# Performance work log

Hardware: AMD Instinct MI355X
Metric: run time of the kernel (lower is better)

The kernel has to match this reference:

```python
import jax, jax.numpy as jnp
import numpy as np

B, I, O, E, K = 32768, 256, 128, 8, 4


def _layernorm(h, g, b, eps=1e-5):
    mu = h.mean(-1, keepdims=True)
    var = h.var(-1, keepdims=True)
    return (h - mu) * jax.lax.rsqrt(var + eps) * g + b


def setup_inputs():
    key = jax.random.key(0)
    ks = iter(jax.random.split(key, 40))
    def w(shape, scale=0.02):
        return jax.random.normal(next(ks), shape, dtype=jnp.float32) * scale
    inp = {
        'x': jax.random.normal(next(ks), (B, I), dtype=jnp.float32),
        'modality_id': jax.random.randint(next(ks), (B,), 0, 3, dtype=jnp.int32),
        # experts 0-1: Linear-ReLU-Linear (stacked over leading expert dim)
        'A_W1': w((2, O, I)), 'A_b1': w((2, O)), 'A_W2': w((2, O, O)), 'A_b2': w((2, O)),
        # experts 2-3: Linear-Tanh-BatchNorm1d(eval)-Linear
        'B_W1': w((2, O, I)), 'B_b1': w((2, O)),
        'B_g': jnp.ones((2, O), jnp.float32), 'B_be': jnp.zeros((2, O), jnp.float32),
        'B_W2': w((2, O, O)), 'B_b2': w((2, O)),
        # experts 4-5: Conv1d(1->4,k3,p1)-Flatten-Linear-GELU
        'C_cw': w((2, 4, 1, 3), 0.1), 'C_cb': w((2, 4)),
        'C_W': w((2, O, 4 * I)), 'C_b': w((2, O)),
        # experts 6-7: Linear-SiLU-LayerNorm-Linear
        'D_W1': w((2, O, I)), 'D_b1': w((2, O)),
        'D_g': jnp.ones((2, O), jnp.float32), 'D_be': jnp.zeros((2, O), jnp.float32),
        'D_W2': w((2, O, O)), 'D_b2': w((2, O)),
        # shared expert: Linear-ReLU-LayerNorm-Linear (dropout off in eval)
        'S_W1': w((O, I)), 'S_b1': w((O,)),
        'S_g': jnp.ones((O,), jnp.float32), 'S_be': jnp.zeros((O,), jnp.float32),
        'S_W2': w((O, O)), 'S_b2': w((O,)),
        # gate: Linear(I+1 -> I//2)-Tanh-Linear(-> E)
        'G_W1': w((I // 2, I + 1)), 'G_b1': w((I // 2,)),
        'G_W2': w((E, I // 2)), 'G_b2': w((E,)),
    }
    return inp


def _forward(x, modality_id, A_W1, A_b1, A_W2, A_b2, B_W1, B_b1, B_g, B_be, B_W2, B_b2,
             C_cw, C_cb, C_W, C_b, D_W1, D_b1, D_g, D_be, D_W2, D_b2,
             S_W1, S_b1, S_g, S_be, S_W2, S_b2, G_W1, G_b1, G_W2, G_b2):
    Bsz = x.shape[0]
    mod = modality_id.astype(x.dtype)[:, None]
    gate_in = jnp.concatenate([x, mod], axis=-1)                 # [B, I+1]
    gh = jnp.tanh(gate_in @ G_W1.T + G_b1)
    logits = jnp.clip((gh @ G_W2.T + G_b2) / 0.7, -10.0, 10.0)   # [B, E]
    topv, topi = jax.lax.top_k(logits, K)
    topw = jax.nn.softmax(topv, axis=-1)                          # [B, K]

    # experts 0-1
    hA = jax.nn.relu(jnp.einsum('bi,eoi->beo', x, A_W1) + A_b1)
    outA = jnp.einsum('beo,epo->bep', hA, A_W2) + A_b2
    # experts 2-3 (BatchNorm eval: running mean 0, var 1)
    hB = jnp.tanh(jnp.einsum('bi,eoi->beo', x, B_W1) + B_b1)
    hB = hB * jax.lax.rsqrt(jnp.asarray(1.0 + 1e-5, x.dtype)) * B_g + B_be
    outB = jnp.einsum('beo,epo->bep', hB, B_W2) + B_b2
    # experts 4-5
    xc = x[:, None, :]                                            # [B,1,I]
    outC = []
    for e in range(2):
        conv = jax.lax.conv_general_dilated(
            xc, C_cw[e], (1,), [(1, 1)],
            dimension_numbers=('NCH', 'OIH', 'NCH')) + C_cb[e][None, :, None]  # [B,4,I]
        flat = conv.reshape(Bsz, 4 * x.shape[1])
        outC.append(jax.nn.gelu(flat @ C_W[e].T + C_b[e], approximate=False))
    outC = jnp.stack(outC, axis=1)
    # experts 6-7
    hD = jax.nn.silu(jnp.einsum('bi,eoi->beo', x, D_W1) + D_b1)
    hD = _layernorm(hD, D_g, D_be)
    outD = jnp.einsum('beo,epo->bep', hD, D_W2) + D_b2

    expert_outputs = jnp.concatenate([outA, outB, outC, outD], axis=1)  # [B,E,O]
    picked = jnp.take_along_axis(expert_outputs, topi[:, :, None], axis=1)  # [B,K,O]
    private = jnp.sum(topw[:, :, None] * picked, axis=1)                # [B,O]

    hS = jax.nn.relu(x @ S_W1.T + S_b1)
    hS = _layernorm(hS, S_g, S_be)
    shared = hS @ S_W2.T + S_b2                                         # [B,O]

    usage = jax.nn.softmax(logits, axis=-1).mean(0)                     # [E]
    ideal = jnp.full_like(usage, 1.0 / E)
    # F.kl_div(log(usage+1e-10), ideal, reduction='batchmean') with N=E
    aux = jnp.mean(ideal * (jnp.log(ideal) - jnp.log(usage + 1e-10)))
    return shared, private, aux


def reference(x, modality_id, A_W1, A_b1, A_W2, A_b2, B_W1, B_b1, B_g, B_be, B_W2, B_b2,
              C_cw, C_cb, C_W, C_b, D_W1, D_b1, D_g, D_be, D_W2, D_b2,
              S_W1, S_b1, S_g, S_be, S_W2, S_b2, G_W1, G_b1, G_W2, G_b2):
    return _forward(x, modality_id, A_W1, A_b1, A_W2, A_b2, B_W1, B_b1, B_g, B_be, B_W2, B_b2,
                    C_cw, C_cb, C_W, C_b, D_W1, D_b1, D_g, D_be, D_W2, D_b2,
                    S_W1, S_b1, S_g, S_be, S_W2, S_b2, G_W1, G_b1, G_W2, G_b2)
```

## Files before the change

### kernel.cpp

```cpp
#include <hip/hip_runtime.h>
#include <hip/hip_bf16.h>
#include <math.h>

typedef __attribute__((ext_vector_type(8))) short short8;
typedef __attribute__((ext_vector_type(4))) float f32x4;
typedef __attribute__((ext_vector_type(4))) unsigned short us4;

#define MFMA16(a,b,c) __builtin_amdgcn_mfma_f32_16x16x32_bf16((a),(b),(c),0,0,0)

#define OFF_W1CAT   0u
#define OFF_W2CAT   589824u
#define OFF_B1      950272u
#define OFF_B2      954880u
#define OFF_LNG     958464u
#define OFF_LNB     960000u
#define OFF_BSC     961536u
#define OFF_BBI     962560u
#define OFF_USAGE   963584u
#define OFF_W8      963712u
#define OFF_W1T     2012288u

__device__ __forceinline__ unsigned short f2bf(float f) {
  union { float f; unsigned u; } v; v.f = f;
  return (unsigned short)((v.u + 0x7fffu + ((v.u >> 16) & 1u)) >> 16);
}
__device__ __forceinline__ float frcp(float x) { return __builtin_amdgcn_rcpf(x); }
__device__ __forceinline__ float ftanh(float x) {
  float ax = fabsf(x);
  float t = __expf(-2.f * ax);
  float r = (1.f - t) * frcp(1.f + t);
  return copysignf(r, x);
}
__device__ __forceinline__ float fsilu(float x) {
  return x * frcp(1.f + __expf(-x));
}
__device__ __forceinline__ float fgelu(float x) {
  float ax = fabsf(x) * 0.70710678118654752f;
  float t = frcp(fmaf(0.3275911f, ax, 1.f));
  float p = fmaf(t, 1.061405429f, -1.453152027f);
  p = fmaf(t, p, 1.421413741f);
  p = fmaf(t, p, -0.284496736f);
  p = fmaf(t, p, 0.254829592f);
  p *= t;
  float erfv = copysignf(fmaf(-p, __expf(-ax * ax), 1.f), x);
  return 0.5f * x * (1.f + erfv);
}

__global__ __launch_bounds__(256) void prep_kernel(
    const float* __restrict__ A_W1, const float* __restrict__ A_b1,
    const float* __restrict__ A_W2, const float* __restrict__ A_b2,
    const float* __restrict__ B_W1, const float* __restrict__ B_b1,
    const float* __restrict__ B_g,  const float* __restrict__ B_be,
    const float* __restrict__ B_W2, const float* __restrict__ B_b2,
    const float* __restrict__ C_cw, const float* __restrict__ C_cb,
    const float* __restrict__ C_W,  const float* __restrict__ C_b,
    const float* __restrict__ D_W1, const float* __restrict__ D_b1,
    const float* __restrict__ D_g,  const float* __restrict__ D_be,
    const float* __restrict__ D_W2, const float* __restrict__ D_b2,
    const float* __restrict__ S_W1, const float* __restrict__ S_b1,
    const float* __restrict__ S_g,  const float* __restrict__ S_be,
    const float* __restrict__ S_W2, const float* __restrict__ S_b2,
    const float* __restrict__ G_W1,
    unsigned short* __restrict__ W1cat, unsigned short* __restrict__ W2cat,
    float* __restrict__ W1T,
    float* __restrict__ b1cat, float* __restrict__ b2cat,
    float* __restrict__ lng, float* __restrict__ lnb,
    float* __restrict__ bsc, float* __restrict__ bbi,
    float* __restrict__ usage)
{
  int tid = blockIdx.x * 256 + threadIdx.x;
  if (tid < 294912) {
    int g = tid >> 15, rem = tid & 32767;
    int j = rem & 7, lane = (rem >> 3) & 63, nt = (rem >> 9) & 7, ks = rem >> 12;
    int p = nt * 16 + (lane & 15);
    int k = ks * 32 + (lane >> 4) * 8 + j;
    int src = p * 256 + k;
    float v;
    if (g < 2)      v = A_W1[g * 32768 + src];
    else if (g < 4) v = B_W1[(g - 2) * 32768 + src];
    else if (g < 6) {
      int e = g - 4;
      v = 0.f;
      for (int c = 0; c < 4; ++c)
        for (int jj = 0; jj < 3; ++jj) {
          int h = k + 1 - jj;
          if (h >= 0 && h < 256)
            v += C_cw[e*12 + c*3 + jj] * C_W[e*131072 + p*1024 + c*256 + h];
        }
    }
    else if (g < 8) v = D_W1[(g - 6) * 32768 + src];
    else            v = S_W1[src];
    W1cat[tid] = f2bf(v);
    return;
  }
  tid -= 294912;
  if (tid < 114688) {
    int g = tid >> 14, rem = tid & 16383;
    int j = rem & 7, lane = (rem >> 3) & 63, nt = (rem >> 9) & 7, ks = rem >> 12;
    int p = nt * 16 + (lane & 15);
    int k = ks * 32 + (lane >> 4) * 8 + j;
    int src = p * 128 + k;
    float v;
    if (g < 2)      v = A_W2[g * 16384 + src];
    else if (g < 4) v = B_W2[(g - 2) * 16384 + src];
    else if (g < 6) v = D_W2[(g - 4) * 16384 + src];
    else            v = S_W2[src];
    W2cat[tid] = f2bf(v);
    return;
  }
  tid -= 114688;
  if (tid < 32896) {
    int k = tid / 128, o = tid % 128;
    W1T[tid] = G_W1[o * 257 + k];
    return;
  }
  tid -= 32896;
  if (tid < 1152) {
    int g = tid / 128, p = tid % 128;
    float v;
    if (g < 2)      v = A_b1[tid];
    else if (g < 4) v = B_b1[p + (g - 2) * 128];
    else if (g < 6) v = C_b[(g - 4) * 128 + p];
    else if (g < 8) v = D_b1[p + (g - 6) * 128];
    else            v = S_b1[p];
    b1cat[tid] = v;
    return;
  }
  tid -= 1152;
  if (tid < 896) {
    int g = tid / 128, p = tid % 128;
    float v;
    if (g < 2)      v = A_b2[tid];
    else if (g < 4) v = B_b2[p + (g - 2) * 128];
    else if (g < 6) v = D_b2[p + (g - 4) * 128];
    else            v = S_b2[p];
    b2cat[tid] = v;
    return;
  }
  tid -= 896;
  if (tid < 768) {
    if (tid < 384) {
      int j = tid / 128, p = tid % 128;
      lng[tid] = (j < 2) ? D_g[tid] : S_g[p];
    } else {
      int q = tid - 384; int j = q / 128, p = q % 128;
      lnb[q] = (j < 2) ? D_be[q] : S_be[p];
    }
    return;
  }
  tid -= 768;
  if (tid < 512) {
    if (tid < 256) bsc[tid] = B_g[tid];
    else           bbi[tid - 256] = B_be[tid - 256];
    return;
  }
  tid -= 512;
  if (tid < 8) usage[tid] = 0.f;
}

__global__ __launch_bounds__(256) void prep2_kernel(
    const float* __restrict__ C_cw_unused, const float* __restrict__ C_cb,
    const float* __restrict__ C_W, float* __restrict__ b1cat)
{
  int tid = blockIdx.x * 256 + threadIdx.x;
  int e = tid >> 9, rem = tid & 511;
  int p = rem >> 2, c = rem & 3;
  const float4* row = (const float4*)(C_W + e*131072 + p*1024 + c*256);
  float s = 0.f;
  for (int q = 0; q < 64; ++q) {
    float4 v = row[q];
    s += v.x + v.y + v.z + v.w;
  }
  atomicAdd(&b1cat[(4 + e) * 128 + p], C_cb[e * 4 + c] * s);
}

__global__ __launch_bounds__(512) void gate_np_kernel(
    const float* __restrict__ x, const int* __restrict__ modality,
    const float* __restrict__ W1T, const float* __restrict__ G_b1,
    const float* __restrict__ G_W2, const float* __restrict__ G_b2,
    float* __restrict__ w8full, float* __restrict__ usage)
{
  __shared__ unsigned char Ubuf[33024];
  __shared__ float ws2[8][132];
  __shared__ float lgs[64][9];
  float* xs  = (float*)Ubuf;
  float* ghs = (float*)Ubuf;
  const int tid = threadIdx.x;
  const int wv = __builtin_amdgcn_readfirstlane(tid >> 6);
  const int lane = tid & 63;
  const int tb = blockIdx.x * 64;
  const int o0 = wv * 16;
  const int t = lane;

  for (int i = tid; i < 1024; i += 512) ws2[i >> 7][i & 127] = G_W2[i];

  float acc[16];
#pragma unroll
  for (int j = 0; j < 16; ++j) acc[j] = 0.f;

  for (int p = 0; p < 2; ++p) {
    __syncthreads();
#pragma unroll
    for (int it = 0; it < 4; ++it) {
      int f = it * 512 + tid;
      int tt = f >> 5, c4 = f & 31;
      int kk = c4 * 4;
      const float4 v = *(const float4*)(x + (size_t)(tb + tt) * 256 + p * 128 + kk);
      int col = tt ^ (((kk >> 4) & 7) << 3);
      xs[(kk + 0) * 64 + col] = v.x;
      xs[(kk + 1) * 64 + col] = v.y;
      xs[(kk + 2) * 64 + col] = v.z;
      xs[(kk + 3) * 64 + col] = v.w;
    }
    __syncthreads();
    const float* wbase = W1T + (size_t)(p * 128) * 128 + o0;
    for (int kk = 0; kk < 128; ++kk) {
      float xv = xs[kk * 64 + (t ^ (((kk >> 4) & 7) << 3))];
      const float* wk = wbase + (size_t)kk * 128;
#pragma unroll
      for (int j = 0; j < 16; ++j)
        acc[j] = fmaf(xv, wk[j], acc[j]);
    }
  }
  {
    float xv = (float)modality[tb + t];
    const float* wk = W1T + (size_t)256 * 128 + o0;
#pragma unroll
    for (int j = 0; j < 16; ++j)
      acc[j] = fmaf(xv, wk[j], acc[j]);
  }
  __syncthreads();
#pragma unroll
  for (int j = 0; j < 16; ++j)
    ghs[t * 129 + o0 + j] = (float)tanh((double)(acc[j] + G_b1[o0 + j]));
  __syncthreads();

  {
    int t2 = tid >> 3, e2 = tid & 7;
    float lg = 0.f;
    for (int o2 = 0; o2 < 128; ++o2)
      lg = fmaf(ghs[t2 * 129 + o2], ws2[e2][o2], lg);
    float s = (lg + G_b2[e2]) / 0.7f;
    lgs[t2][e2] = fminf(fmaxf(s, -10.f), 10.f);
  }
  __syncthreads();

  if (wv == 0) {
    int token = tb + lane;
    float v[8];
#pragma unroll
    for (int e = 0; e < 8; ++e) v[e] = lgs[lane][e];
    float tv[4]; int ti[4]; unsigned msk = 0;
    for (int kk = 0; kk < 4; ++kk) {
      float best = -1e30f; int bi = 0;
      for (int e = 0; e < 8; ++e)
        if (!((msk >> e) & 1u) && v[e] > best) { best = v[e]; bi = e; }
      tv[kk] = best; ti[kk] = bi; msk |= 1u << bi;
    }
    float mx = tv[0], den = 0.f, wk4[4];
#pragma unroll
    for (int kk = 0; kk < 4; ++kk) { wk4[kk] = expf(tv[kk] - mx); den += wk4[kk]; }
#pragma unroll
    for (int e = 0; e < 8; ++e) {
      float val = 0.f;
#pragma unroll
      for (int kk = 0; kk < 4; ++kk) if (ti[kk] == e) val = wk4[kk] / den;
      w8full[(size_t)token * 8 + e] = val;
    }
    float uw[8];
    float dall = 0.f, pe[8];
#pragma unroll
    for (int e = 0; e < 8; ++e) { pe[e] = expf(v[e] - mx); dall += pe[e]; }
#pragma unroll
    for (int e = 0; e < 8; ++e) uw[e] = pe[e] / dall;
    for (int m = 1; m <= 32; m <<= 1)
#pragma unroll
      for (int e = 0; e < 8; ++e) uw[e] += __shfl_xor(uw[e], m);
    if (lane == 0)
      for (int e = 0; e < 8; ++e) atomicAdd(usage + e, uw[e]);
  }
}

__global__ __launch_bounds__(512, 2) void moe_kernel(
    const float* __restrict__ x,
    const unsigned short* __restrict__ W1cat, const unsigned short* __restrict__ W2cat,
    const float* __restrict__ b1cat, const float* __restrict__ b2cat,
    const float* __restrict__ lng, const float* __restrict__ lnb,
    const float* __restrict__ bsc, const float* __restrict__ bbi,
    const float* __restrict__ w8full, float* __restrict__ out)
{
  __shared__ unsigned char smem[131072];
  short8* W1L = (short8*)smem;
  short8* W2L = (short8*)(smem + 65536);
  unsigned char* HS = smem + 98304 + (threadIdx.x >> 6) * 4096;

  const int tid = threadIdx.x;
  const int wv = tid >> 6, lane = tid & 63;
  const int l15 = lane & 15, l4 = lane >> 4;
  const int tb = blockIdx.x * 128 + wv * 16;
  const short8* W1f = (const short8*)W1cat;
  const short8* W2f = (const short8*)W2cat;

  short8 A[8];
#pragma unroll
  for (int ks = 0; ks < 8; ++ks) {
    const float* xr = x + (size_t)(tb + l15) * 256 + ks * 32 + l4 * 8;
    float4 u = *(const float4*)xr, v = *(const float4*)(xr + 4);
    short8 a;
    a[0]=(short)f2bf(u.x); a[1]=(short)f2bf(u.y); a[2]=(short)f2bf(u.z); a[3]=(short)f2bf(u.w);
    a[4]=(short)f2bf(v.x); a[5]=(short)f2bf(v.y); a[6]=(short)f2bf(v.z); a[7]=(short)f2bf(v.w);
    A[ks] = a;
  }

  f32x4 zero = {0.f, 0.f, 0.f, 0.f};
  f32x4 pacc[8];
#pragma unroll
  for (int nt = 0; nt < 8; ++nt) pacc[nt] = zero;
  const float RS = 1.0f / sqrtf(1.0f + 1e-5f);

  short8 stg[12];
#pragma unroll
  for (int i = 0; i < 8; ++i) stg[i] = W1f[tid + i * 512];
#pragma unroll
  for (int i = 0; i < 4; ++i) stg[8 + i] = W2f[tid + i * 512];

  for (int g = 0; g < 9; ++g) {
    const int type = (g < 2) ? 0 : (g < 4) ? 1 : (g < 6) ? 2 : (g < 8) ? 3 : 4;
    const int g2 = (g < 4) ? g : ((g == 8) ? 6 : g - 2);

    __syncthreads();
#pragma unroll
    for (int i = 0; i < 8; ++i) W1L[tid + i * 512] = stg[i];
#pragma unroll
    for (int i = 0; i < 4; ++i) W2L[tid + i * 512] = stg[8 + i];
    if (g < 8) {
      int gn = g + 1;
      int g2n = (gn < 4) ? gn : ((gn == 8) ? 6 : gn - 2);
#pragma unroll
      for (int i = 0; i < 8; ++i) stg[i] = W1f[(size_t)gn * 4096 + tid + i * 512];
#pragma unroll
      for (int i = 0; i < 4; ++i) stg[8 + i] = W2f[(size_t)g2n * 2048 + tid + i * 512];
    }
    __syncthreads();

    f32x4 acc[8];
#pragma unroll
    for (int nt = 0; nt < 8; ++nt) acc[nt] = zero;
#pragma unroll
    for (int ks = 0; ks < 8; ++ks)
#pragma unroll
      for (int nt = 0; nt < 8; ++nt)
        acc[nt] = MFMA16(A[ks], W1L[(ks * 8 + nt) * 64 + lane], acc[nt]);

    const float* b1 = b1cat + g * 128;

    if (type == 2) {
#pragma unroll
      for (int r = 0; r < 4; ++r) {
        float wv_ = w8full[(size_t)(tb + l4 * 4 + r) * 8 + g];
#pragma unroll
        for (int nt = 0; nt < 8; ++nt) {
          float h = fgelu(acc[nt][r] + b1[nt * 16 + l15]);
          pacc[nt][r] += wv_ * h;
        }
      }
      continue;
    }
#pragma unroll
    for (int r = 0; r < 4; ++r)
#pragma unroll
      for (int nt = 0; nt < 8; ++nt) {
        float h = acc[nt][r] + b1[nt * 16 + l15];
        if (type == 0)      h = fmaxf(h, 0.f);
        else if (type == 1) {
          int col = (g - 2) * 128 + nt * 16 + l15;
          h = ftanh(h) * RS * bsc[col] + bbi[col];
        }
        else if (type == 3) h = fsilu(h);
        else                h = fmaxf(h, 0.f);
        acc[nt][r] = h;
      }
    if (type >= 3) {
      int li = (type == 4) ? 2 : (g - 6);
#pragma unroll
      for (int r = 0; r < 4; ++r) {
        float s1 = 0.f, s2 = 0.f;
#pragma unroll
        for (int nt = 0; nt < 8; ++nt) { float h = acc[nt][r]; s1 += h; s2 += h * h; }
        for (int m = 1; m <= 8; m <<= 1) { s1 += __shfl_xor(s1, m); s2 += __shfl_xor(s2, m); }
        float mu = s1 * (1.f / 128.f);
        float var = s2 * (1.f / 128.f) - mu * mu;
        float sc = __builtin_amdgcn_rsqf(var + 1e-5f);
#pragma unroll
        for (int nt = 0; nt < 8; ++nt) {
          int col = nt * 16 + l15;
          acc[nt][r] = (acc[nt][r] - mu) * sc * lng[li * 128 + col] + lnb[li * 128 + col];
        }
      }
    }
#pragma unroll
    for (int r = 0; r < 4; ++r) {
      int row = l4 * 4 + r;
#pragma unroll
      for (int nt = 0; nt < 8; ++nt) {
        int bytecol = (nt * 16 + l15) * 2;
        int addr = row * 256 + ((((bytecol >> 4) ^ (row & 7)) << 4) | (bytecol & 15));
        *(unsigned short*)(HS + addr) = f2bf(acc[nt][r]);
      }
    }
    short8 a2[4];
#pragma unroll
    for (int ks = 0; ks < 4; ++ks) {
      int ar = l15 * 256 + ((((ks * 4 + l4) ^ (l15 & 7)) << 4));
      a2[ks] = *(const short8*)(HS + ar);
    }
    f32x4 acc2[8];
#pragma unroll
    for (int nt = 0; nt < 8; ++nt) acc2[nt] = zero;
#pragma unroll
    for (int ks = 0; ks < 4; ++ks)
#pragma unroll
      for (int nt = 0; nt < 8; ++nt)
        acc2[nt] = MFMA16(a2[ks], W2L[(ks * 8 + nt) * 64 + lane], acc2[nt]);

    const float* b2 = b2cat + g2 * 128;
    if (type == 4) {
#pragma unroll
      for (int r = 0; r < 4; ++r) {
        int token = tb + l4 * 4 + r;
#pragma unroll
        for (int nt = 0; nt < 8; ++nt)
          out[(size_t)token * 128 + nt * 16 + l15] = acc2[nt][r] + b2[nt * 16 + l15];
      }
    } else {
#pragma unroll
      for (int r = 0; r < 4; ++r) {
        float wv_ = w8full[(size_t)(tb + l4 * 4 + r) * 8 + g];
#pragma unroll
        for (int nt = 0; nt < 8; ++nt)
          pacc[nt][r] += wv_ * (acc2[nt][r] + b2[nt * 16 + l15]);
      }
    }
  }
#pragma unroll
  for (int r = 0; r < 4; ++r) {
    int token = tb + l4 * 4 + r;
#pragma unroll
    for (int nt = 0; nt < 8; ++nt)
      out[4194304 + (size_t)token * 128 + nt * 16 + l15] = pacc[nt][r];
  }
}

__global__ void aux_kernel(const float* __restrict__ usage, float* __restrict__ out) {
  if (threadIdx.x == 0 && blockIdx.x == 0) {
    float a = 0.f;
    for (int e = 0; e < 8; ++e) {
      float u = usage[e] * (1.0f / 32768.0f);
      a += 0.125f * (logf(0.125f) - logf(u + 1e-10f));
    }
    out[8388608] = a * 0.125f;
  }
}

extern "C" void kernel_launch(void* const* d_in, const int* in_sizes, int n_in,
                              void* d_out, int out_size, void* d_ws, size_t ws_size,
                              hipStream_t stream) {
  (void)in_sizes; (void)n_in; (void)out_size; (void)ws_size;
  const float* x    = (const float*)d_in[0];
  const int*   mod  = (const int*)d_in[1];
  const float* A_W1 = (const float*)d_in[2];
  const float* A_b1 = (const float*)d_in[3];
  const float* A_W2 = (const float*)d_in[4];
  const float* A_b2 = (const float*)d_in[5];
  const float* B_W1 = (const float*)d_in[6];
  const float* B_b1 = (const float*)d_in[7];
  const float* B_g  = (const float*)d_in[8];
  const float* B_be = (const float*)d_in[9];
  const float* B_W2 = (const float*)d_in[10];
  const float* B_b2 = (const float*)d_in[11];
  const float* C_cw = (const float*)d_in[12];
  const float* C_cb = (const float*)d_in[13];
  const float* C_W  = (const float*)d_in[14];
  const float* C_b  = (const float*)d_in[15];
  const float* D_W1 = (const float*)d_in[16];
  const float* D_b1 = (const float*)d_in[17];
  const float* D_g  = (const float*)d_in[18];
  const float* D_be = (const float*)d_in[19];
  const float* D_W2 = (const float*)d_in[20];
  const float* D_b2 = (const float*)d_in[21];
  const float* S_W1 = (const float*)d_in[22];
  const float* S_b1 = (const float*)d_in[23];
  const float* S_g  = (const float*)d_in[24];
  const float* S_be = (const float*)d_in[25];
  const float* S_W2 = (const float*)d_in[26];
  const float* S_b2 = (const float*)d_in[27];
  const float* G_W1 = (const float*)d_in[28];
  const float* G_b1 = (const float*)d_in[29];
  const float* G_W2 = (const float*)d_in[30];
  const float* G_b2 = (const float*)d_in[31];

  char* ws = (char*)d_ws;
  unsigned short* W1cat = (unsigned short*)(ws + OFF_W1CAT);
  unsigned short* W2cat = (unsigned short*)(ws + OFF_W2CAT);
  float* W1T    = (float*)(ws + OFF_W1T);
  float* b1cat  = (float*)(ws + OFF_B1);
  float* b2cat  = (float*)(ws + OFF_B2);
  float* lng    = (float*)(ws + OFF_LNG);
  float* lnb    = (float*)(ws + OFF_LNB);
  float* bsc    = (float*)(ws + OFF_BSC);
  float* bbi    = (float*)(ws + OFF_BBI);
  float* usage  = (float*)(ws + OFF_USAGE);
  float* w8full = (float*)(ws + OFF_W8);
  float* out    = (float*)d_out;

  prep_kernel<<<1742, 256, 0, stream>>>(A_W1, A_b1, A_W2, A_b2, B_W1, B_b1, B_g, B_be,
      B_W2, B_b2, C_cw, C_cb, C_W, C_b, D_W1, D_b1, D_g, D_be, D_W2, D_b2,
      S_W1, S_b1, S_g, S_be, S_W2, S_b2, G_W1,
      W1cat, W2cat, W1T, b1cat, b2cat, lng, lnb, bsc, bbi, usage);
  prep2_kernel<<<4, 256, 0, stream>>>(C_cw, C_cb, C_W, b1cat);
  gate_np_kernel<<<512, 512, 0, stream>>>(x, mod, W1T, G_b1, G_W2, G_b2,
      w8full, usage);
  moe_kernel<<<256, 512, 0, stream>>>(x, W1cat, W2cat, b1cat, b2cat, lng, lnb,
      bsc, bbi, w8full, out);
  aux_kernel<<<1, 64, 0, stream>>>(usage, out);
}
```

Before: 220.6 us.

## Compute gate layer with split-bf16 MFMA and exact fp32 fallback for near-ties

Replaces the scalar fp32 FMA gate first layer with MFMA using a three-term bf16 hi/lo split of both x and the gate weights, which approximates fp32 accuracy. Tokens whose 4th and 5th logits lie within a small margin are flagged and recomputed on the exact fp32 path, so top-k selection should match the reference. Prep gains a pass that packs the split gate weights, and the gate kernel now uses about 144KB of LDS with 128 tokens per block. The risks are lower occupancy and the extra cost of the per-token fallback loop.

```diff
diff --git a/kernel.cpp b/kernel.cpp
--- a/kernel.cpp
+++ b/kernel.cpp
@@ -19,16 +19,29 @@
 #define OFF_USAGE   963584u
 #define OFF_W8      963712u
 #define OFF_W1T     2012288u
+#define OFF_GW1HF   2143872u
+#define OFF_GW1LF   2209408u
+
+#define DELTA 2e-3f
 
 __device__ __forceinline__ unsigned short f2bf(float f) {
   union { float f; unsigned u; } v; v.f = f;
   return (unsigned short)((v.u + 0x7fffu + ((v.u >> 16) & 1u)) >> 16);
+}
+__device__ __forceinline__ float bf2f(unsigned short b) {
+  union { unsigned u; float f; } v; v.u = ((unsigned)b) << 16; return v.f;
 }
 __device__ __forceinline__ float frcp(float x) { return __builtin_amdgcn_rcpf(x); }
 __device__ __forceinline__ float ftanh(float x) {
   float ax = fabsf(x);
   float t = __expf(-2.f * ax);
   float r = (1.f - t) * frcp(1.f + t);
+  return copysignf(r, x);
+}
+__device__ __forceinline__ float ftanh_acc(float x) {
+  float ax = fabsf(x);
+  float t = __expf(-2.f * ax);
+  float r = (1.f - t) / (1.f + t);
   return copysignf(r, x);
 }
 __device__ __forceinline__ float fsilu(float x) {
@@ -63,6 +76,7 @@
     const float* __restrict__ G_W1,
     unsigned short* __restrict__ W1cat, unsigned short* __restrict__ W2cat,
     float* __restrict__ W1T,
+    unsigned short* __restrict__ GW1HF, unsigned short* __restrict__ GW1LF,
     float* __restrict__ b1cat, float* __restrict__ b2cat,
     float* __restrict__ lng, float* __restrict__ lnb,
     float* __restrict__ bsc, float* __restrict__ bbi,
@@ -115,6 +129,17 @@
     return;
   }
   tid -= 32896;
+  if (tid < 32768) {
+    int j = tid & 7, lane = (tid >> 3) & 63, nt = (tid >> 9) & 7, ks = tid >> 12;
+    int o = nt * 16 + (lane & 15);
+    int k = ks * 32 + (lane >> 4) * 8 + j;
+    float v = G_W1[o * 257 + k];
+    unsigned short h = f2bf(v);
+    GW1HF[tid] = h;
+    GW1LF[tid] = f2bf(v - bf2f(h));
+    return;
+  }
+  tid -= 32768;
   if (tid < 1152) {
     int g = tid / 128, p = tid % 128;
     float v;
@@ -174,110 +199,201 @@
   atomicAdd(&b1cat[(4 + e) * 128 + p], C_cb[e * 4 + c] * s);
 }
 
-__global__ __launch_bounds__(512) void gate_np_kernel(
+__global__ __launch_bounds__(512, 2) void gate_kernel(
     const float* __restrict__ x, const int* __restrict__ modality,
-    const float* __restrict__ W1T, const float* __restrict__ G_b1,
-    const float* __restrict__ G_W2, const float* __restrict__ G_b2,
+    const unsigned short* __restrict__ GW1HF, const unsigned short* __restrict__ GW1LF,
+    const float* __restrict__ W1T, const float* __restrict__ G_W1,
+    const float* __restrict__ G_b1, const float* __restrict__ G_W2,
+    const float* __restrict__ G_b2,
     float* __restrict__ w8full, float* __restrict__ usage)
 {
-  __shared__ unsigned char Ubuf[33024];
-  __shared__ float ws2[8][132];
-  __shared__ float lgs[64][9];
-  float* xs  = (float*)Ubuf;
-  float* ghs = (float*)Ubuf;
+  __shared__ unsigned char smem[147520];
+  short8* BhL   = (short8*)smem;
+  short8* BlL   = (short8*)(smem + 65536);
+  float*  ws2   = (float*)(smem + 131072);
+  float*  ghsl  = (float*)(smem + 135168);
+  float*  xsl   = (float*)(smem + 139264);
+  unsigned* flagw = (unsigned*)(smem + 147456);
+
   const int tid = threadIdx.x;
-  const int wv = __builtin_amdgcn_readfirstlane(tid >> 6);
-  const int lane = tid & 63;
-  const int tb = blockIdx.x * 64;
-  const int o0 = wv * 16;
-  const int t = lane;
-
-  for (int i = tid; i < 1024; i += 512) ws2[i >> 7][i & 127] = G_W2[i];
-
-  float acc[16];
-#pragma unroll
-  for (int j = 0; j < 16; ++j) acc[j] = 0.f;
-
-  for (int p = 0; p < 2; ++p) {
-    __syncthreads();
-#pragma unroll
-    for (int it = 0; it < 4; ++it) {
-      int f = it * 512 + tid;
-      int tt = f >> 5, c4 = f & 31;
-      int kk = c4 * 4;
-      const float4 v = *(const float4*)(x + (size_t)(tb + tt) * 256 + p * 128 + kk);
-      int col = tt ^ (((kk >> 4) & 7) << 3);
-      xs[(kk + 0) * 64 + col] = v.x;
-      xs[(kk + 1) * 64 + col] = v.y;
-      xs[(kk + 2) * 64 + col] = v.z;
-      xs[(kk + 3) * 64 + col] = v.w;
-    }
-    __syncthreads();
-    const float* wbase = W1T + (size_t)(p * 128) * 128 + o0;
-    for (int kk = 0; kk < 128; ++kk) {
-      float xv = xs[kk * 64 + (t ^ (((kk >> 4) & 7) << 3))];
-      const float* wk = wbase + (size_t)kk * 128;
-#pragma unroll
-      for (int j = 0; j < 16; ++j)
-        acc[j] = fmaf(xv, wk[j], acc[j]);
-    }
-  }
-  {
-    float xv = (float)modality[tb + t];
-    const float* wk = W1T + (size_t)256 * 128 + o0;
-#pragma unroll
-    for (int j = 0; j < 16; ++j)
-      acc[j] = fmaf(xv, wk[j], acc[j]);
+  const int wv = tid >> 6, lane = tid & 63;
+  const int l15 = lane & 15, l4 = lane >> 4;
+  const int tbw = blockIdx.x * 128 + wv * 16;
+
+  const short8* srcH = (const short8*)GW1HF;
+  const short8* srcL = (const short8*)GW1LF;
+#pragma unroll
+  for (int i = 0; i < 8; ++i) BhL[tid + i * 512] = srcH[tid + i * 512];
+#pragma unroll
+  for (int i = 0; i < 8; ++i) BlL[tid + i * 512] = srcL[tid + i * 512];
+  for (int i = tid; i < 1024; i += 512) ws2[i] = G_W2[i];
+  if (lane == 0) flagw[wv] = 0;
+
+  short8 XH[8], XL[8];
+#pragma unroll
+  for (int ks = 0; ks < 8; ++ks) {
+    const float* xr = x + (size_t)(tbw + l15) * 256 + ks * 32 + l4 * 8;
+    float4 u = *(const float4*)xr, v = *(const float4*)(xr + 4);
+    float xv[8] = {u.x, u.y, u.z, u.w, v.x, v.y, v.z, v.w};
+    short8 hh, ll;
+#pragma unroll
+    for (int j2 = 0; j2 < 8; ++j2) {
+      unsigned short h = f2bf(xv[j2]);
+      hh[j2] = (short)h;
+      ll[j2] = (short)f2bf(xv[j2] - bf2f(h));
+    }
+    XH[ks] = hh; XL[ks] = ll;
   }
   __syncthreads();
-#pragma unroll
-  for (int j = 0; j < 16; ++j)
-    ghs[t * 129 + o0 + j] = (float)tanh((double)(acc[j] + G_b1[o0 + j]));
-  __syncthreads();
-
-  {
-    int t2 = tid >> 3, e2 = tid & 7;
+
+  f32x4 zero = {0.f, 0.f, 0.f, 0.f};
+  f32x4 acc[8];
+#pragma unroll
+  for (int nt = 0; nt < 8; ++nt) acc[nt] = zero;
+#pragma unroll
+  for (int ks = 0; ks < 8; ++ks) {
+#pragma unroll
+    for (int nt = 0; nt < 8; ++nt) {
+      short8 bh = BhL[(ks * 8 + nt) * 64 + lane];
+      short8 bl = BlL[(ks * 8 + nt) * 64 + lane];
+      acc[nt] = MFMA16(XH[ks], bh, acc[nt]);
+      acc[nt] = MFMA16(XH[ks], bl, acc[nt]);
+      acc[nt] = MFMA16(XL[ks], bh, acc[nt]);
+    }
+  }
+  float mf[4];
+#pragma unroll
+  for (int r = 0; r < 4; ++r) mf[r] = (float)modality[tbw + l4 * 4 + r];
+  float ghreg[8][4];
+#pragma unroll
+  for (int nt = 0; nt < 8; ++nt) {
+    int o = nt * 16 + l15;
+    float wm = G_W1[o * 257 + 256];
+    float b = G_b1[o];
+#pragma unroll
+    for (int r = 0; r < 4; ++r)
+      ghreg[nt][r] = ftanh_acc(fmaf(mf[r], wm, acc[nt][r]) + b);
+  }
+  float part[8][4];
+#pragma unroll
+  for (int e = 0; e < 8; ++e) {
+    float w[8];
+#pragma unroll
+    for (int nt = 0; nt < 8; ++nt) w[nt] = ws2[e * 128 + nt * 16 + l15];
+#pragma unroll
+    for (int r = 0; r < 4; ++r) {
+      float s = 0.f;
+#pragma unroll
+      for (int nt = 0; nt < 8; ++nt) s = fmaf(ghreg[nt][r], w[nt], s);
+      part[e][r] = s;
+    }
+  }
+#pragma unroll
+  for (int m = 1; m <= 8; m <<= 1)
+#pragma unroll
+    for (int e = 0; e < 8; ++e)
+#pragma unroll
+      for (int r = 0; r < 4; ++r)
+        part[e][r] += __shfl_xor(part[e][r], m);
+
+  float uw[8];
+#pragma unroll
+  for (int e = 0; e < 8; ++e) uw[e] = 0.f;
+  if (l15 == 0) {
+    for (int r = 0; r < 4; ++r) {
+      int token = tbw + l4 * 4 + r;
+      float v[8];
+#pragma unroll
+      for (int e = 0; e < 8; ++e)
+        v[e] = fminf(fmaxf((part[e][r] + G_b2[e]) / 0.7f, -10.f), 10.f);
+      float tv[5]; int ti[5]; unsigned msk = 0;
+      for (int kk = 0; kk < 5; ++kk) {
+        float best = -1e30f; int bi = 0;
+        for (int e = 0; e < 8; ++e)
+          if (!((msk >> e) & 1u) && v[e] > best) { best = v[e]; bi = e; }
+        tv[kk] = best; ti[kk] = bi; msk |= 1u << bi;
+      }
+      if (tv[3] - tv[4] < DELTA) {
+        atomicOr(&flagw[wv], 1u << (l4 * 4 + r));
+      } else {
+        float mx = tv[0], den = 0.f, wk4[4];
+#pragma unroll
+        for (int kk = 0; kk < 4; ++kk) { wk4[kk] = expf(tv[kk] - mx); den += wk4[kk]; }
+#pragma unroll
+        for (int e = 0; e < 8; ++e) {
+          float val = 0.f;
+#pragma unroll
+          for (int kk = 0; kk < 4; ++kk) if (ti[kk] == e) val = wk4[kk] / den;
+          w8full[(size_t)token * 8 + e] = val;
+        }
+        float dall = 0.f, pe[8];
+#pragma unroll
+        for (int e = 0; e < 8; ++e) { pe[e] = expf(v[e] - mx); dall += pe[e]; }
+#pragma unroll
+        for (int e = 0; e < 8; ++e) uw[e] += pe[e] / dall;
+      }
+    }
+  }
+#pragma unroll
+  for (int m = 16; m <= 32; m <<= 1)
+#pragma unroll
+    for (int e = 0; e < 8; ++e) uw[e] += __shfl_xor(uw[e], m);
+  if (lane == 0)
+    for (int e = 0; e < 8; ++e) atomicAdd(usage + e, uw[e]);
+
+  unsigned fl = flagw[wv];
+  while (fl) {
+    int t = __builtin_ctz(fl); fl &= fl - 1;
+    int T = tbw + t;
+#pragma unroll
+    for (int q = 0; q < 4; ++q)
+      xsl[wv * 256 + q * 64 + lane] = x[(size_t)T * 256 + q * 64 + lane];
+    float a0 = 0.f, a1 = 0.f;
+    for (int k = 0; k < 256; ++k) {
+      float xv = xsl[wv * 256 + k];
+      a0 = fmaf(xv, W1T[k * 128 + lane], a0);
+      a1 = fmaf(xv, W1T[k * 128 + 64 + lane], a1);
+    }
+    {
+      float xv = (float)modality[T];
+      a0 = fmaf(xv, W1T[256 * 128 + lane], a0);
+      a1 = fmaf(xv, W1T[256 * 128 + 64 + lane], a1);
+    }
+    ghsl[wv * 128 + lane]      = (float)tanh((double)(a0 + G_b1[lane]));
+    ghsl[wv * 128 + 64 + lane] = (float)tanh((double)(a1 + G_b1[64 + lane]));
     float lg = 0.f;
-    for (int o2 = 0; o2 < 128; ++o2)
-      lg = fmaf(ghs[t2 * 129 + o2], ws2[e2][o2], lg);
-    float s = (lg + G_b2[e2]) / 0.7f;
-    lgs[t2][e2] = fminf(fmaxf(s, -10.f), 10.f);
-  }
-  __syncthreads();
-
-  if (wv == 0) {
-    int token = tb + lane;
+    if (lane < 8)
+      for (int o = 0; o < 128; ++o)
+        lg = fmaf(ghsl[wv * 128 + o], ws2[lane * 128 + o], lg);
     float v[8];
 #pragma unroll
-    for (int e = 0; e < 8; ++e) v[e] = lgs[lane][e];
-    float tv[4]; int ti[4]; unsigned msk = 0;
-    for (int kk = 0; kk < 4; ++kk) {
-      float best = -1e30f; int bi = 0;
+    for (int e = 0; e < 8; ++e) v[e] = __shfl(lg, e);
+    if (lane == 0) {
+#pragma unroll
       for (int e = 0; e < 8; ++e)
-        if (!((msk >> e) & 1u) && v[e] > best) { best = v[e]; bi = e; }
-      tv[kk] = best; ti[kk] = bi; msk |= 1u << bi;
-    }
-    float mx = tv[0], den = 0.f, wk4[4];
-#pragma unroll
-    for (int kk = 0; kk < 4; ++kk) { wk4[kk] = expf(tv[kk] - mx); den += wk4[kk]; }
-#pragma unroll
-    for (int e = 0; e < 8; ++e) {
-      float val = 0.f;
-#pragma unroll
-      for (int kk = 0; kk < 4; ++kk) if (ti[kk] == e) val = wk4[kk] / den;
-      w8full[(size_t)token * 8 + e] = val;
-    }
-    float uw[8];
-    float dall = 0.f, pe[8];
-#pragma unroll
-    for (int e = 0; e < 8; ++e) { pe[e] = expf(v[e] - mx); dall += pe[e]; }
-#pragma unroll
-    for (int e = 0; e < 8; ++e) uw[e] = pe[e] / dall;
-    for (int m = 1; m <= 32; m <<= 1)
-#pragma unroll
-      for (int e = 0; e < 8; ++e) uw[e] += __shfl_xor(uw[e], m);
-    if (lane == 0)
-      for (int e = 0; e < 8; ++e) atomicAdd(usage + e, uw[e]);
+        v[e] = fminf(fmaxf((v[e] + G_b2[e]) / 0.7f, -10.f), 10.f);
+      float tv[4]; int ti[4]; unsigned msk = 0;
+      for (int kk = 0; kk < 4; ++kk) {
+        float best = -1e30f; int bi = 0;
+        for (int e = 0; e < 8; ++e)
+          if (!((msk >> e) & 1u) && v[e] > best) { best = v[e]; bi = e; }
+        tv[kk] = best; ti[kk] = bi; msk |= 1u << bi;
+      }
+      float mx = tv[0], den = 0.f, wk4[4];
+#pragma unroll
+      for (int kk = 0; kk < 4; ++kk) { wk4[kk] = expf(tv[kk] - mx); den += wk4[kk]; }
+#pragma unroll
+      for (int e = 0; e < 8; ++e) {
+        float val = 0.f;
+#pragma unroll
+        for (int kk = 0; kk < 4; ++kk) if (ti[kk] == e) val = wk4[kk] / den;
+        w8full[(size_t)T * 8 + e] = val;
+      }
+      float dall = 0.f, pe[8];
+#pragma unroll
+      for (int e = 0; e < 8; ++e) { pe[e] = expf(v[e] - mx); dall += pe[e]; }
+      for (int e = 0; e < 8; ++e) atomicAdd(usage + e, pe[e] / dall);
+    }
   }
 }
 
@@ -503,6 +619,8 @@
   unsigned short* W1cat = (unsigned short*)(ws + OFF_W1CAT);
   unsigned short* W2cat = (unsigned short*)(ws + OFF_W2CAT);
   float* W1T    = (float*)(ws + OFF_W1T);
+  unsigned short* GW1HF = (unsigned short*)(ws + OFF_GW1HF);
+  unsigned short* GW1LF = (unsigned short*)(ws + OFF_GW1LF);
   float* b1cat  = (float*)(ws + OFF_B1);
   float* b2cat  = (float*)(ws + OFF_B2);
   float* lng    = (float*)(ws + OFF_LNG);
@@ -513,13 +631,13 @@
   float* w8full = (float*)(ws + OFF_W8);
   float* out    = (float*)d_out;
 
-  prep_kernel<<<1742, 256, 0, stream>>>(A_W1, A_b1, A_W2, A_b2, B_W1, B_b1, B_g, B_be,
+  prep_kernel<<<1870, 256, 0, stream>>>(A_W1, A_b1, A_W2, A_b2, B_W1, B_b1, B_g, B_be,
       B_W2, B_b2, C_cw, C_cb, C_W, C_b, D_W1, D_b1, D_g, D_be, D_W2, D_b2,
       S_W1, S_b1, S_g, S_be, S_W2, S_b2, G_W1,
-      W1cat, W2cat, W1T, b1cat, b2cat, lng, lnb, bsc, bbi, usage);
+      W1cat, W2cat, W1T, GW1HF, GW1LF, b1cat, b2cat, lng, lnb, bsc, bbi, usage);
   prep2_kernel<<<4, 256, 0, stream>>>(C_cw, C_cb, C_W, b1cat);
-  gate_np_kernel<<<512, 512, 0, stream>>>(x, mod, W1T, G_b1, G_W2, G_b2,
-      w8full, usage);
+  gate_kernel<<<256, 512, 0, stream>>>(x, mod, GW1HF, GW1LF, W1T, G_W1,
+      G_b1, G_W2, G_b2, w8full, usage);
   moe_kernel<<<256, 512, 0, stream>>>(x, W1cat, W2cat, b1cat, b2cat, lng, lnb,
       bsc, bbi, w8full, out);
   aux_kernel<<<1, 64, 0, stream>>>(usage, out);
```

New measurement: 541.2 us. +145.3%, slower.
